# Performance work log

Hardware: AMD Instinct MI355X
Metric: run time of the kernel (lower is better)

Reference implementation:

```python
import jax, jax.numpy as jnp
import numpy as np

N = 100000   # nodes
E = 1600000  # edges
D = 128      # input_dim
H = 128      # hidden_dim
O = 128      # output_dim
G = 64       # graphs in batch
BN_EPS = 1e-5


def setup_inputs() -> dict:
    key = jax.random.key(0)
    ks = jax.random.split(key, 32)
    x = jax.random.normal(ks[0], (N, D), jnp.float32)
    edge_index = jax.random.randint(ks[1], (2, E), 0, N, dtype=jnp.int64)
    batch = jnp.sort(jax.random.randint(ks[2], (N,), 0, G, dtype=jnp.int64))

    def lin_w(k, fan_in, fan_out):
        return (jax.random.normal(k, (fan_in, fan_out), jnp.float32) / np.sqrt(fan_in)).astype(jnp.float32)

    def lin_b(k, fan_out):
        return (0.01 * jax.random.normal(k, (fan_out,), jnp.float32)).astype(jnp.float32)

    def bn(k, dim):
        k1, k2, k3, k4 = jax.random.split(k, 4)
        gamma = 1.0 + 0.1 * jax.random.normal(k1, (dim,), jnp.float32)
        beta = 0.1 * jax.random.normal(k2, (dim,), jnp.float32)
        mean = 0.1 * jax.random.normal(k3, (dim,), jnp.float32)
        var = 0.5 + jax.random.uniform(k4, (dim,), jnp.float32)
        return gamma, beta, mean, var

    inp = {
        "x": x, "edge_index": edge_index, "batch": batch,
        "w11": lin_w(ks[3], D, H), "b11": lin_b(ks[4], H),
        "w12": lin_w(ks[5], H, H), "b12": lin_b(ks[6], H),
        "w21": lin_w(ks[7], H, H), "b21": lin_b(ks[8], H),
        "w22": lin_w(ks[9], H, H), "b22": lin_b(ks[10], H),
        "w31": lin_w(ks[11], H, H), "b31": lin_b(ks[12], H),
        "w32": lin_w(ks[13], H, O), "b32": lin_b(ks[14], O),
    }
    g1, be1, m1, v1 = bn(ks[15], H)
    g2, be2, m2, v2 = bn(ks[16], H)
    g3, be3, m3, v3 = bn(ks[17], O)
    inp.update({"bn1_g": g1, "bn1_b": be1, "bn1_m": m1, "bn1_v": v1,
                "bn2_g": g2, "bn2_b": be2, "bn2_m": m2, "bn2_v": v2,
                "bn3_g": g3, "bn3_b": be3, "bn3_m": m3, "bn3_v": v3})
    return inp


def _gin_conv(x, src, dst, wa, ba, wb, bb):
    # sum-aggregate neighbor features: out[i] = x[i] + sum_{(j->i) in E} x[j]  (eps=0)
    agg = jax.ops.segment_sum(x[src], dst, num_segments=N)
    h = x + agg
    # 2-layer MLP: Linear -> ReLU -> Linear
    return jax.nn.relu(h @ wa + ba) @ wb + bb


def _bn_eval(x, g, b, m, v):
    return (x - m) * (g * jax.lax.rsqrt(v + BN_EPS)) + b


def reference(x, edge_index, batch,
              w11, b11, w12, b12, w21, b21, w22, b22, w31, b31, w32, b32,
              bn1_g, bn1_b, bn1_m, bn1_v,
              bn2_g, bn2_b, bn2_m, bn2_v,
              bn3_g, bn3_b, bn3_m, bn3_v):
    src, dst = edge_index[0], edge_index[1]
    h = _gin_conv(x, src, dst, w11, b11, w12, b12)
    h = jax.nn.relu(_bn_eval(h, bn1_g, bn1_b, bn1_m, bn1_v))  # dropout: eval-mode identity
    h = _gin_conv(h, src, dst, w21, b21, w22, b22)
    h = jax.nn.relu(_bn_eval(h, bn2_g, bn2_b, bn2_m, bn2_v))
    h = _gin_conv(h, src, dst, w31, b31, w32, b32)
    h = jax.nn.relu(_bn_eval(h, bn3_g, bn3_b, bn3_m, bn3_v))
    # global mean pool over each graph
    sums = jax.ops.segment_sum(h, batch, num_segments=G)
    counts = jax.ops.segment_sum(jnp.ones((N,), h.dtype), batch, num_segments=G)
    return sums / jnp.maximum(counts, 1.0)[:, None]
```

## Files before the change

kernel.cpp:

```cpp
#include <hip/hip_runtime.h>
#include <hip/hip_bf16.h>
#include <cstdint>

static constexpr int D = 128;
static constexpr int SPANB = 9;
static constexpr int CHUNK = 4096;

typedef __bf16 v8bf __attribute__((ext_vector_type(8)));
typedef float  v4f  __attribute__((ext_vector_type(4)));

__device__ inline float bflo(unsigned u) { return __uint_as_float(u << 16); }
__device__ inline float bfhi(unsigned u) { return __uint_as_float(u & 0xffff0000u); }
__device__ inline unsigned short bfbits(float f) {
    __hip_bfloat16 h = __float2bfloat16(f);
    return *reinterpret_cast<unsigned short*>(&h);
}
__device__ inline unsigned packbf(float a, float b) {
    return (unsigned)bfbits(a) | ((unsigned)bfbits(b) << 16);
}

__global__ __launch_bounds__(256) void prep_kernel(
    const float* __restrict__ w11, const float* __restrict__ w12,
    const float* __restrict__ w21, const float* __restrict__ w22,
    const float* __restrict__ w31, const float* __restrict__ w32,
    __hip_bfloat16* __restrict__ Wp,
    const float* bn1g, const float* bn1b, const float* bn1m, const float* bn1v, const float* lb1,
    const float* bn2g, const float* bn2b, const float* bn2m, const float* bn2v, const float* lb2,
    const float* bn3g, const float* bn3b, const float* bn3m, const float* bn3v, const float* lb3,
    float* sc1, float* sh1, float* sc2, float* sh2, float* sc3, float* sh3,
    const float* __restrict__ x, __hip_bfloat16* __restrict__ xb, long long n8,
    const int* __restrict__ dst, int* __restrict__ blockhist, int nE, int nblk) {
    int b = blockIdx.x, t = threadIdx.x;
    if (b < 48) {
        int idx = b * 256 + t;
        int widx = idx >> 11, r = idx & 2047;
        const float* W = widx == 0 ? w11 : widx == 1 ? w12 : widx == 2 ? w21
                       : widx == 3 ? w22 : widx == 4 ? w31 : w32;
        int l = r & 63, cf = (r >> 6) & 7, ks = r >> 9;
        int k0 = ks * 32 + (l >> 4) * 8, c = cf * 16 + (l & 15);
        unsigned o0 = packbf(W[(k0 + 0) * D + c], W[(k0 + 1) * D + c]);
        unsigned o1 = packbf(W[(k0 + 2) * D + c], W[(k0 + 3) * D + c]);
        unsigned o2 = packbf(W[(k0 + 4) * D + c], W[(k0 + 5) * D + c]);
        unsigned o3 = packbf(W[(k0 + 6) * D + c], W[(k0 + 7) * D + c]);
        reinterpret_cast<uint4*>(Wp + (size_t)idx * 8)[0] = make_uint4(o0, o1, o2, o3);
    } else if (b < 51) {
        if (t < D) {
            int j = b - 48;
            const float *g, *bb, *m, *v, *lb;
            float *sc, *sh;
            if (j == 0)      { g = bn1g; bb = bn1b; m = bn1m; v = bn1v; lb = lb1; sc = sc1; sh = sh1; }
            else if (j == 1) { g = bn2g; bb = bn2b; m = bn2m; v = bn2v; lb = lb2; sc = sc2; sh = sh2; }
            else             { g = bn3g; bb = bn3b; m = bn3m; v = bn3v; lb = lb3; sc = sc3; sh = sh3; }
            float s = g[t] * rsqrtf(v[t] + 1e-5f);
            sc[t] = s;
            sh[t] = (lb[t] - m[t]) * s + bb[t];
        }
    } else if (b < 51 + nblk) {
        __shared__ int h[256];
        h[t] = 0;
        __syncthreads();
        int base = (b - 51) * CHUNK;
#pragma unroll
        for (int i = 0; i < CHUNK / 256; ++i) {
            int e = base + i * 256 + t;
            if (e < nE) atomicAdd(&h[dst[e] >> SPANB], 1);
        }
        __syncthreads();
        blockhist[(b - 51) * 256 + t] = h[t];
    } else {
        long long i = (long long)(b - 51 - nblk) * 256 + t;
        if (i < n8) {
            const float4* f4 = reinterpret_cast<const float4*>(x);
            float4 a = f4[i * 2], bb = f4[i * 2 + 1];
            uint4 o = make_uint4(packbf(a.x, a.y), packbf(a.z, a.w),
                                 packbf(bb.x, bb.y), packbf(bb.z, bb.w));
            reinterpret_cast<uint4*>(xb)[i] = o;
        }
    }
}

__global__ __launch_bounds__(256) void bscan_kernel(int* __restrict__ blockhist,
                                                    int* __restrict__ totals, int nblk) {
    __shared__ int s[256];
    int b = blockIdx.x, t = threadIdx.x;
    int running = 0;
    for (int base = 0; base < nblk; base += 256) {
        int idx = base + t;
        int v = (idx < nblk) ? blockhist[idx * 256 + b] : 0;
        s[t] = v;
        __syncthreads();
#pragma unroll
        for (int off = 1; off < 256; off <<= 1) {
            int add = (t >= off) ? s[t - off] : 0;
            __syncthreads();
            s[t] += add;
            __syncthreads();
        }
        if (idx < nblk) blockhist[idx * 256 + b] = running + s[t] - v;
        int tot = s[255];
        __syncthreads();
        running += tot;
    }
    if (t == 0) totals[b] = running;
}

__global__ void tscan_kernel(const int* __restrict__ totals,
                             int* __restrict__ bucketbase, int nbuk, int nE) {
    __shared__ int s[256];
    int t = threadIdx.x;
    int v = (t < nbuk) ? totals[t] : 0;
    s[t] = v;
    __syncthreads();
#pragma unroll
    for (int off = 1; off < 256; off <<= 1) {
        int add = (t >= off) ? s[t - off] : 0;
        __syncthreads();
        s[t] += add;
        __syncthreads();
    }
    if (t < nbuk) bucketbase[t] = s[t] - v;
    if (t == 0) bucketbase[nbuk] = nE;
}

__global__ __launch_bounds__(256) void fill2_kernel(const int* __restrict__ src,
                                                    const int* __restrict__ dst,
                                                    const int* __restrict__ blockhist,
                                                    const int* __restrict__ bucketbase,
                                                    unsigned* __restrict__ records,
                                                    int nE, int nbuk) {
    __shared__ int cur[256];
    int t = threadIdx.x;
    if (t < nbuk) cur[t] = bucketbase[t] + blockhist[blockIdx.x * 256 + t];
    __syncthreads();
    int base = blockIdx.x * CHUNK;
#pragma unroll
    for (int i = 0; i < CHUNK / 256; ++i) {
        int e = base + i * 256 + t;
        if (e < nE) {
            int d = dst[e], s = src[e];
            int p = atomicAdd(&cur[d >> SPANB], 1);
            records[p] = ((unsigned)s << SPANB) | (unsigned)(d & ((1 << SPANB) - 1));
        }
    }
}

__global__ __launch_bounds__(512) void csr2_kernel(const unsigned* __restrict__ records,
                                                   const int* __restrict__ bucketbase,
                                                   int* __restrict__ rowptr,
                                                   int* __restrict__ col,
                                                   int nN, int nE) {
    __shared__ int cnt[512];
    __shared__ int cur[512];
    int b = blockIdx.x, t = threadIdx.x;
    int node0 = b << SPANB;
    cnt[t] = 0;
    __syncthreads();
    int rbeg = bucketbase[b], rend = bucketbase[b + 1];
    for (int r = rbeg + t; r < rend; r += 512)
        atomicAdd(&cnt[records[r] & ((1 << SPANB) - 1)], 1);
    __syncthreads();
    int v = cnt[t];
#pragma unroll
    for (int off = 1; off < 512; off <<= 1) {
        int add = (t >= off) ? cnt[t - off] : 0;
        __syncthreads();
        cnt[t] += add;
        __syncthreads();
    }
    int pos = rbeg + cnt[t] - v;
    if (node0 + t < nN) rowptr[node0 + t] = pos;
    if (b == 0 && t == 0) rowptr[nN] = nE;
    cur[t] = pos;
    __syncthreads();
    for (int r = rbeg + t; r < rend; r += 512) {
        unsigned rec = records[r];
        int p = atomicAdd(&cur[rec & ((1 << SPANB) - 1)], 1);
        col[p] = (int)(rec >> SPANB);
    }
}

#define ACC8(vv) { a[0]+=bflo(vv.x); a[1]+=bfhi(vv.x); a[2]+=bflo(vv.y); a[3]+=bfhi(vv.y); \
                   a[4]+=bflo(vv.z); a[5]+=bfhi(vv.z); a[6]+=bflo(vv.w); a[7]+=bfhi(vv.w); }

__global__ __launch_bounds__(256) void agg_kernel(const __hip_bfloat16* __restrict__ h,
                                                  __hip_bfloat16* __restrict__ S,
                                                  const int* __restrict__ rowptr,
                                                  const int* __restrict__ col, int nN) {
    int node = blockIdx.x * 16 + (threadIdx.x >> 4);
    if (node >= nN) return;
    int q = threadIdx.x & 15;
    const uint4* h4 = reinterpret_cast<const uint4*>(h);
    uint4 u = h4[(size_t)node * 16 + q];
    float a[8];
    a[0] = bflo(u.x); a[1] = bfhi(u.x); a[2] = bflo(u.y); a[3] = bfhi(u.y);
    a[4] = bflo(u.z); a[5] = bfhi(u.z); a[6] = bflo(u.w); a[7] = bfhi(u.w);
    int beg = rowptr[node], end = rowptr[node + 1];
    int j = beg;
    for (; j + 3 < end; j += 4) {
        int s0 = col[j], s1 = col[j + 1], s2 = col[j + 2], s3 = col[j + 3];
        uint4 v0 = h4[(size_t)s0 * 16 + q];
        uint4 v1 = h4[(size_t)s1 * 16 + q];
        uint4 v2 = h4[(size_t)s2 * 16 + q];
        uint4 v3 = h4[(size_t)s3 * 16 + q];
        ACC8(v0); ACC8(v1); ACC8(v2); ACC8(v3);
    }
    for (; j < end; ++j) {
        uint4 v0 = h4[(size_t)col[j] * 16 + q];
        ACC8(v0);
    }
    uint4 o = make_uint4(packbf(a[0], a[1]), packbf(a[2], a[3]),
                         packbf(a[4], a[5]), packbf(a[6], a[7]));
    reinterpret_cast<uint4*>(S)[(size_t)node * 16 + q] = o;
}

__global__ __launch_bounds__(256) void mlp_fused_kernel(
    const __hip_bfloat16* __restrict__ A,
    const __hip_bfloat16* __restrict__ WpA,
    const __hip_bfloat16* __restrict__ WpB,
    const float* __restrict__ b1,
    const float* __restrict__ sc, const float* __restrict__ sh,
    __hip_bfloat16* __restrict__ out, int nN) {
    __shared__ __attribute__((aligned(16))) char smem[4][8192];
    int w = threadIdx.x >> 6, l = threadIdx.x & 63;
    int q = l >> 4, r16 = l & 15;
    int row0 = blockIdx.x * 128 + w * 32;
    int rowA = row0 + r16, rowB = row0 + 16 + r16;
    int arA = rowA < nN ? rowA : nN - 1;
    int arB = rowB < nN ? rowB : nN - 1;
    const v8bf* ArA = reinterpret_cast<const v8bf*>(A + (size_t)arA * D);
    const v8bf* ArB = reinterpret_cast<const v8bf*>(A + (size_t)arB * D);
    const v8bf* Wa = reinterpret_cast<const v8bf*>(WpA);
    const v8bf* Wb = reinterpret_cast<const v8bf*>(WpB);
    const float4* b14 = reinterpret_cast<const float4*>(b1);
    const float4* sc4 = reinterpret_cast<const float4*>(sc);
    const float4* sh4 = reinterpret_cast<const float4*>(sh);
    char* my = smem[w];
    int swz = (r16 & 7) << 4;

    v4f acc[2][8] = {};
#pragma unroll
    for (int ks = 0; ks < 4; ++ks) {
        v8bf bA = ArA[ks * 4 + q];
        v8bf bB = ArB[ks * 4 + q];
#pragma unroll
        for (int cf = 0; cf < 8; ++cf) {
            v8bf wa = Wa[(ks * 8 + cf) * 64 + l];
            acc[0][cf] = __builtin_amdgcn_mfma_f32_16x16x32_bf16(wa, bA, acc[0][cf], 0, 0, 0);
            acc[1][cf] = __builtin_amdgcn_mfma_f32_16x16x32_bf16(wa, bB, acc[1][cf], 0, 0, 0);
        }
    }
#pragma unroll
    for (int half = 0; half < 2; ++half) {
        char* base = my + half * 4096;
#pragma unroll
        for (int cf = 0; cf < 8; ++cf) {
            float4 bb = b14[cf * 4 + q];
            float e0 = fmaxf(acc[half][cf][0] + bb.x, 0.f);
            float e1 = fmaxf(acc[half][cf][1] + bb.y, 0.f);
            float e2 = fmaxf(acc[half][cf][2] + bb.z, 0.f);
            float e3 = fmaxf(acc[half][cf][3] + bb.w, 0.f);
            int waddr = r16 * 256 + ((cf * 32 + q * 8) ^ swz);
            *reinterpret_cast<uint2*>(base + waddr) = make_uint2(packbf(e0, e1), packbf(e2, e3));
        }
    }
    __syncthreads();

    v4f acc2[2][8] = {};
#pragma unroll
    for (int ks = 0; ks < 4; ++ks) {
        v8bf bA = *reinterpret_cast<v8bf*>(my + r16 * 256 + ((ks * 64 + q * 16) ^ swz));
        v8bf bB = *reinterpret_cast<v8bf*>(my + 4096 + r16 * 256 + ((ks * 64 + q * 16) ^ swz));
#pragma unroll
        for (int cf = 0; cf < 8; ++cf) {
            v8bf wb = Wb[(ks * 8 + cf) * 64 + l];
            acc2[0][cf] = __builtin_amdgcn_mfma_f32_16x16x32_bf16(wb, bA, acc2[0][cf], 0, 0, 0);
            acc2[1][cf] = __builtin_amdgcn_mfma_f32_16x16x32_bf16(wb, bB, acc2[1][cf], 0, 0, 0);
        }
    }
#pragma unroll
    for (int half = 0; half < 2; ++half) {
        int row = (half == 0) ? rowA : rowB;
        if (row < nN) {
#pragma unroll
            for (int cf = 0; cf < 8; ++cf) {
                float4 s0 = sc4[cf * 4 + q], s1 = sh4[cf * 4 + q];
                float e0 = fmaxf(acc2[half][cf][0] * s0.x + s1.x, 0.f);
                float e1 = fmaxf(acc2[half][cf][1] * s0.y + s1.y, 0.f);
                float e2 = fmaxf(acc2[half][cf][2] * s0.z + s1.z, 0.f);
                float e3 = fmaxf(acc2[half][cf][3] * s0.w + s1.w, 0.f);
                *reinterpret_cast<uint2*>(out + (size_t)row * D + cf * 16 + q * 4) =
                    make_uint2(packbf(e0, e1), packbf(e2, e3));
            }
        }
    }
}

__global__ __launch_bounds__(1024) void pool2_kernel(const __hip_bfloat16* __restrict__ h,
                                                     const int* __restrict__ batch,
                                                     float* __restrict__ out, int nN) {
    int g = blockIdx.x;
    int lo, hi;
    {
        int a = 0, b = nN;
        while (a < b) { int mid = (a + b) >> 1; if (batch[mid] < g) a = mid + 1; else b = mid; }
        lo = a;
        b = nN;
        while (a < b) { int mid = (a + b) >> 1; if (batch[mid] < g + 1) a = mid + 1; else b = mid; }
        hi = a;
    }
    int grp = threadIdx.x >> 4;
    int q = threadIdx.x & 15;
    float a[8] = {};
    const uint4* h4 = reinterpret_cast<const uint4*>(h);
    for (int i = lo + grp; i < hi; i += 64) {
        uint4 v = h4[(size_t)i * 16 + q];
        ACC8(v);
    }
    __shared__ float red[64][130];
#pragma unroll
    for (int k = 0; k < 8; ++k) red[grp][q * 8 + k] = a[k];
    __syncthreads();
    int t = threadIdx.x;
    if (t < D) {
        float s = 0.f;
#pragma unroll 8
        for (int r = 0; r < 64; ++r) s += red[r][t];
        out[(size_t)g * D + t] = s / fmaxf((float)(hi - lo), 1.f);
    }
}

extern "C" void kernel_launch(void* const* d_in, const int* in_sizes, int n_in,
                              void* d_out, int out_size, void* d_ws, size_t ws_size,
                              hipStream_t stream) {
    const float* x    = (const float*)d_in[0];
    const int*   ei   = (const int*)d_in[1];
    const int*   batch= (const int*)d_in[2];
    const float* w11 = (const float*)d_in[3];  const float* b11 = (const float*)d_in[4];
    const float* w12 = (const float*)d_in[5];  const float* b12 = (const float*)d_in[6];
    const float* w21 = (const float*)d_in[7];  const float* b21 = (const float*)d_in[8];
    const float* w22 = (const float*)d_in[9];  const float* b22 = (const float*)d_in[10];
    const float* w31 = (const float*)d_in[11]; const float* b31 = (const float*)d_in[12];
    const float* w32 = (const float*)d_in[13]; const float* b32 = (const float*)d_in[14];
    const float* bn1g = (const float*)d_in[15]; const float* bn1b = (const float*)d_in[16];
    const float* bn1m = (const float*)d_in[17]; const float* bn1v = (const float*)d_in[18];
    const float* bn2g = (const float*)d_in[19]; const float* bn2b = (const float*)d_in[20];
    const float* bn2m = (const float*)d_in[21]; const float* bn2v = (const float*)d_in[22];
    const float* bn3g = (const float*)d_in[23]; const float* bn3b = (const float*)d_in[24];
    const float* bn3m = (const float*)d_in[25]; const float* bn3v = (const float*)d_in[26];

    int nN = in_sizes[0] / D;
    int nE = in_sizes[1] / 2;
    int nG = out_size / D;

    const int* srcp = ei;
    const int* dstp = ei + nE;

    size_t NB2 = (size_t)nN * D * sizeof(__hip_bfloat16);
    char* ws = (char*)d_ws;
    __hip_bfloat16* S16 = (__hip_bfloat16*)ws;
    __hip_bfloat16* M16 = (__hip_bfloat16*)(ws + NB2);
    __hip_bfloat16* P16 = (__hip_bfloat16*)(ws + 2 * NB2);
    __hip_bfloat16* Wp  = (__hip_bfloat16*)(ws + 3 * NB2);
    size_t wp_bytes = 6 * 2048 * 8 * sizeof(__hip_bfloat16);
    char* auxp = ws + 3 * NB2 + wp_bytes;
    size_t aux_bytes = 16384;
    float* sc1 = (float*)auxp + 0,   *sh1 = (float*)auxp + 128;
    float* sc2 = (float*)auxp + 256, *sh2 = (float*)auxp + 384;
    float* sc3 = (float*)auxp + 512, *sh3 = (float*)auxp + 640;
    int*   bucketbase = (int*)(auxp + (768 + 64) * 4);
    int*   totals     = bucketbase + 300;
    int* rowptr = (int*)(auxp + aux_bytes);
    int* col    = rowptr + (nN + 1);

    unsigned* records = (unsigned*)M16;
    int* blockhist    = (int*)((char*)M16 + (size_t)nE * 4);

    int nbuk = (nN + 511) >> SPANB;
    int nblk = (nE + CHUNK - 1) / CHUNK;
    long long n8 = (long long)nN * D / 8;
    int cvtBlocks = (int)((n8 + 255) / 256);

    prep_kernel<<<51 + nblk + cvtBlocks, 256, 0, stream>>>(
        w11, w12, w21, w22, w31, w32, Wp,
        bn1g, bn1b, bn1m, bn1v, b12,
        bn2g, bn2b, bn2m, bn2v, b22,
        bn3g, bn3b, bn3m, bn3v, b32,
        sc1, sh1, sc2, sh2, sc3, sh3,
        x, (__hip_bfloat16*)P16, n8,
        dstp, blockhist, nE, nblk);

    bscan_kernel<<<nbuk, 256, 0, stream>>>(blockhist, totals, nblk);
    tscan_kernel<<<1, 256, 0, stream>>>(totals, bucketbase, nbuk, nE);
    fill2_kernel<<<nblk, 256, 0, stream>>>(srcp, dstp, blockhist, bucketbase, records, nE, nbuk);
    csr2_kernel<<<nbuk, 512, 0, stream>>>(records, bucketbase, rowptr, col, nN, nE);

    int mlpBlocks = (nN + 127) / 128;
    int aggBlocks = (nN + 15) / 16;
    __hip_bfloat16* Wp1 = Wp + 0 * 16384; __hip_bfloat16* Wp2 = Wp + 1 * 16384;
    __hip_bfloat16* Wp3 = Wp + 2 * 16384; __hip_bfloat16* Wp4 = Wp + 3 * 16384;
    __hip_bfloat16* Wp5 = Wp + 4 * 16384; __hip_bfloat16* Wp6 = Wp + 5 * 16384;

    agg_kernel<<<aggBlocks, 256, 0, stream>>>(P16, S16, rowptr, col, nN);
    mlp_fused_kernel<<<mlpBlocks, 256, 0, stream>>>(S16, Wp1, Wp2, b11, sc1, sh1, P16, nN);

    agg_kernel<<<aggBlocks, 256, 0, stream>>>(P16, S16, rowptr, col, nN);
    mlp_fused_kernel<<<mlpBlocks, 256, 0, stream>>>(S16, Wp3, Wp4, b21, sc2, sh2, P16, nN);

    agg_kernel<<<aggBlocks, 256, 0, stream>>>(P16, S16, rowptr, col, nN);
    mlp_fused_kernel<<<mlpBlocks, 256, 0, stream>>>(S16, Wp5, Wp6, b31, sc3, sh3, P16, nN);

    pool2_kernel<<<nG, 1024, 0, stream>>>(P16, batch, (float*)d_out, nN);
}
```

Baseline: 346.6 us.

## Fuse neighbor aggregation and MLP into one per-layer kernel via LDS

Merges the gather-sum aggregation kernel and the two-layer MLP kernel into one layer kernel. Each block aggregates 64 nodes into swizzled shared memory, then runs both MFMA GEMMs on that tile, so the aggregated bf16 tensor is never written to or reread from global memory. The cost is fewer rows per wave (16 instead of 32), which halves weight-fragment reuse, plus extra barriers. The gather phase also now shares a block with MFMA work, which could lower the number of loads in flight.

```diff
diff --git a/kernel.cpp b/kernel.cpp
--- a/kernel.cpp
+++ b/kernel.cpp
@@ -182,115 +182,109 @@
 #define ACC8(vv) { a[0]+=bflo(vv.x); a[1]+=bfhi(vv.x); a[2]+=bflo(vv.y); a[3]+=bfhi(vv.y); \
                    a[4]+=bflo(vv.z); a[5]+=bfhi(vv.z); a[6]+=bflo(vv.w); a[7]+=bfhi(vv.w); }
 
-__global__ __launch_bounds__(256) void agg_kernel(const __hip_bfloat16* __restrict__ h,
-                                                  __hip_bfloat16* __restrict__ S,
-                                                  const int* __restrict__ rowptr,
-                                                  const int* __restrict__ col, int nN) {
-    int node = blockIdx.x * 16 + (threadIdx.x >> 4);
-    if (node >= nN) return;
-    int q = threadIdx.x & 15;
-    const uint4* h4 = reinterpret_cast<const uint4*>(h);
-    uint4 u = h4[(size_t)node * 16 + q];
-    float a[8];
-    a[0] = bflo(u.x); a[1] = bfhi(u.x); a[2] = bflo(u.y); a[3] = bfhi(u.y);
-    a[4] = bflo(u.z); a[5] = bfhi(u.z); a[6] = bflo(u.w); a[7] = bfhi(u.w);
-    int beg = rowptr[node], end = rowptr[node + 1];
-    int j = beg;
-    for (; j + 3 < end; j += 4) {
-        int s0 = col[j], s1 = col[j + 1], s2 = col[j + 2], s3 = col[j + 3];
-        uint4 v0 = h4[(size_t)s0 * 16 + q];
-        uint4 v1 = h4[(size_t)s1 * 16 + q];
-        uint4 v2 = h4[(size_t)s2 * 16 + q];
-        uint4 v3 = h4[(size_t)s3 * 16 + q];
-        ACC8(v0); ACC8(v1); ACC8(v2); ACC8(v3);
-    }
-    for (; j < end; ++j) {
-        uint4 v0 = h4[(size_t)col[j] * 16 + q];
-        ACC8(v0);
-    }
-    uint4 o = make_uint4(packbf(a[0], a[1]), packbf(a[2], a[3]),
-                         packbf(a[4], a[5]), packbf(a[6], a[7]));
-    reinterpret_cast<uint4*>(S)[(size_t)node * 16 + q] = o;
-}
-
-__global__ __launch_bounds__(256) void mlp_fused_kernel(
-    const __hip_bfloat16* __restrict__ A,
-    const __hip_bfloat16* __restrict__ WpA,
-    const __hip_bfloat16* __restrict__ WpB,
+__global__ __launch_bounds__(256) void layer_kernel(
+    const __hip_bfloat16* __restrict__ Hin,
+    const int* __restrict__ rowptr, const int* __restrict__ col,
+    const __hip_bfloat16* __restrict__ WpA, const __hip_bfloat16* __restrict__ WpB,
     const float* __restrict__ b1,
     const float* __restrict__ sc, const float* __restrict__ sh,
-    __hip_bfloat16* __restrict__ out, int nN) {
-    __shared__ __attribute__((aligned(16))) char smem[4][8192];
-    int w = threadIdx.x >> 6, l = threadIdx.x & 63;
-    int q = l >> 4, r16 = l & 15;
-    int row0 = blockIdx.x * 128 + w * 32;
-    int rowA = row0 + r16, rowB = row0 + 16 + r16;
-    int arA = rowA < nN ? rowA : nN - 1;
-    int arB = rowB < nN ? rowB : nN - 1;
-    const v8bf* ArA = reinterpret_cast<const v8bf*>(A + (size_t)arA * D);
-    const v8bf* ArB = reinterpret_cast<const v8bf*>(A + (size_t)arB * D);
+    __hip_bfloat16* __restrict__ Hout, int nN) {
+    __shared__ __attribute__((aligned(16))) char Sl[64 * 256];
+    int t = threadIdx.x;
+    int row0 = blockIdx.x * 64;
+
+    {
+        int grp = t >> 4, q = t & 15;
+        const uint4* h4 = reinterpret_cast<const uint4*>(Hin);
+#pragma unroll
+        for (int n = 0; n < 4; ++n) {
+            int r = grp * 4 + n;
+            int node = row0 + r;
+            int waddr = r * 256 + ((q * 16) ^ ((r & 7) << 4));
+            if (node >= nN) {
+                *reinterpret_cast<uint4*>(Sl + waddr) = make_uint4(0, 0, 0, 0);
+                continue;
+            }
+            uint4 u = h4[(size_t)node * 16 + q];
+            float a[8];
+            a[0] = bflo(u.x); a[1] = bfhi(u.x); a[2] = bflo(u.y); a[3] = bfhi(u.y);
+            a[4] = bflo(u.z); a[5] = bfhi(u.z); a[6] = bflo(u.w); a[7] = bfhi(u.w);
+            int beg = rowptr[node], end = rowptr[node + 1];
+            int j = beg;
+            for (; j + 3 < end; j += 4) {
+                int s0 = col[j], s1 = col[j + 1], s2 = col[j + 2], s3 = col[j + 3];
+                uint4 v0 = h4[(size_t)s0 * 16 + q];
+                uint4 v1 = h4[(size_t)s1 * 16 + q];
+                uint4 v2 = h4[(size_t)s2 * 16 + q];
+                uint4 v3 = h4[(size_t)s3 * 16 + q];
+                ACC8(v0); ACC8(v1); ACC8(v2); ACC8(v3);
+            }
+            for (; j < end; ++j) {
+                uint4 v0 = h4[(size_t)col[j] * 16 + q];
+                ACC8(v0);
+            }
+            *reinterpret_cast<uint4*>(Sl + waddr) =
+                make_uint4(packbf(a[0], a[1]), packbf(a[2], a[3]),
+                           packbf(a[4], a[5]), packbf(a[6], a[7]));
+        }
+    }
+    __syncthreads();
+
+    int w = t >> 6, l = t & 63;
+    int q2 = l >> 4, r16 = l & 15;
+    int lrow = w * 16 + r16;
+    int row = row0 + lrow;
+    int swz = (r16 & 7) << 4;
+    char* srow = Sl + lrow * 256;
+    char* mid = Sl + w * 4096;
     const v8bf* Wa = reinterpret_cast<const v8bf*>(WpA);
     const v8bf* Wb = reinterpret_cast<const v8bf*>(WpB);
     const float4* b14 = reinterpret_cast<const float4*>(b1);
     const float4* sc4 = reinterpret_cast<const float4*>(sc);
     const float4* sh4 = reinterpret_cast<const float4*>(sh);
-    char* my = smem[w];
-    int swz = (r16 & 7) << 4;
-
-    v4f acc[2][8] = {};
+
+    v4f acc[8] = {};
 #pragma unroll
     for (int ks = 0; ks < 4; ++ks) {
-        v8bf bA = ArA[ks * 4 + q];
-        v8bf bB = ArB[ks * 4 + q];
+        v8bf bfrag = *reinterpret_cast<v8bf*>(srow + (((ks * 4 + q2) * 16) ^ swz));
+#pragma unroll
+        for (int cf = 0; cf < 8; ++cf)
+            acc[cf] = __builtin_amdgcn_mfma_f32_16x16x32_bf16(
+                Wa[(ks * 8 + cf) * 64 + l], bfrag, acc[cf], 0, 0, 0);
+    }
+    __syncthreads();
+
+#pragma unroll
+    for (int cf = 0; cf < 8; ++cf) {
+        float4 bb = b14[cf * 4 + q2];
+        float e0 = fmaxf(acc[cf][0] + bb.x, 0.f);
+        float e1 = fmaxf(acc[cf][1] + bb.y, 0.f);
+        float e2 = fmaxf(acc[cf][2] + bb.z, 0.f);
+        float e3 = fmaxf(acc[cf][3] + bb.w, 0.f);
+        int waddr = r16 * 256 + ((cf * 32 + q2 * 8) ^ swz);
+        *reinterpret_cast<uint2*>(mid + waddr) = make_uint2(packbf(e0, e1), packbf(e2, e3));
+    }
+    __syncthreads();
+
+    v4f acc2[8] = {};
+#pragma unroll
+    for (int ks = 0; ks < 4; ++ks) {
+        v8bf bfrag = *reinterpret_cast<v8bf*>(mid + r16 * 256 + ((ks * 64 + q2 * 16) ^ swz));
+#pragma unroll
+        for (int cf = 0; cf < 8; ++cf)
+            acc2[cf] = __builtin_amdgcn_mfma_f32_16x16x32_bf16(
+                Wb[(ks * 8 + cf) * 64 + l], bfrag, acc2[cf], 0, 0, 0);
+    }
+    if (row < nN) {
 #pragma unroll
         for (int cf = 0; cf < 8; ++cf) {
-            v8bf wa = Wa[(ks * 8 + cf) * 64 + l];
-            acc[0][cf] = __builtin_amdgcn_mfma_f32_16x16x32_bf16(wa, bA, acc[0][cf], 0, 0, 0);
-            acc[1][cf] = __builtin_amdgcn_mfma_f32_16x16x32_bf16(wa, bB, acc[1][cf], 0, 0, 0);
-        }
-    }
-#pragma unroll
-    for (int half = 0; half < 2; ++half) {
-        char* base = my + half * 4096;
-#pragma unroll
-        for (int cf = 0; cf < 8; ++cf) {
-            float4 bb = b14[cf * 4 + q];
-            float e0 = fmaxf(acc[half][cf][0] + bb.x, 0.f);
-            float e1 = fmaxf(acc[half][cf][1] + bb.y, 0.f);
-            float e2 = fmaxf(acc[half][cf][2] + bb.z, 0.f);
-            float e3 = fmaxf(acc[half][cf][3] + bb.w, 0.f);
-            int waddr = r16 * 256 + ((cf * 32 + q * 8) ^ swz);
-            *reinterpret_cast<uint2*>(base + waddr) = make_uint2(packbf(e0, e1), packbf(e2, e3));
-        }
-    }
-    __syncthreads();
-
-    v4f acc2[2][8] = {};
-#pragma unroll
-    for (int ks = 0; ks < 4; ++ks) {
-        v8bf bA = *reinterpret_cast<v8bf*>(my + r16 * 256 + ((ks * 64 + q * 16) ^ swz));
-        v8bf bB = *reinterpret_cast<v8bf*>(my + 4096 + r16 * 256 + ((ks * 64 + q * 16) ^ swz));
-#pragma unroll
-        for (int cf = 0; cf < 8; ++cf) {
-            v8bf wb = Wb[(ks * 8 + cf) * 64 + l];
-            acc2[0][cf] = __builtin_amdgcn_mfma_f32_16x16x32_bf16(wb, bA, acc2[0][cf], 0, 0, 0);
-            acc2[1][cf] = __builtin_amdgcn_mfma_f32_16x16x32_bf16(wb, bB, acc2[1][cf], 0, 0, 0);
-        }
-    }
-#pragma unroll
-    for (int half = 0; half < 2; ++half) {
-        int row = (half == 0) ? rowA : rowB;
-        if (row < nN) {
-#pragma unroll
-            for (int cf = 0; cf < 8; ++cf) {
-                float4 s0 = sc4[cf * 4 + q], s1 = sh4[cf * 4 + q];
-                float e0 = fmaxf(acc2[half][cf][0] * s0.x + s1.x, 0.f);
-                float e1 = fmaxf(acc2[half][cf][1] * s0.y + s1.y, 0.f);
-                float e2 = fmaxf(acc2[half][cf][2] * s0.z + s1.z, 0.f);
-                float e3 = fmaxf(acc2[half][cf][3] * s0.w + s1.w, 0.f);
-                *reinterpret_cast<uint2*>(out + (size_t)row * D + cf * 16 + q * 4) =
-                    make_uint2(packbf(e0, e1), packbf(e2, e3));
-            }
+            float4 s0 = sc4[cf * 4 + q2], s1 = sh4[cf * 4 + q2];
+            float e0 = fmaxf(acc2[cf][0] * s0.x + s1.x, 0.f);
+            float e1 = fmaxf(acc2[cf][1] * s0.y + s1.y, 0.f);
+            float e2 = fmaxf(acc2[cf][2] * s0.z + s1.z, 0.f);
+            float e3 = fmaxf(acc2[cf][3] * s0.w + s1.w, 0.f);
+            *reinterpret_cast<uint2*>(Hout + (size_t)row * D + cf * 16 + q2 * 4) =
+                make_uint2(packbf(e0, e1), packbf(e2, e3));
         }
     }
 }
@@ -357,12 +351,11 @@
 
     size_t NB2 = (size_t)nN * D * sizeof(__hip_bfloat16);
     char* ws = (char*)d_ws;
-    __hip_bfloat16* S16 = (__hip_bfloat16*)ws;
-    __hip_bfloat16* M16 = (__hip_bfloat16*)(ws + NB2);
-    __hip_bfloat16* P16 = (__hip_bfloat16*)(ws + 2 * NB2);
-    __hip_bfloat16* Wp  = (__hip_bfloat16*)(ws + 3 * NB2);
+    __hip_bfloat16* A16 = (__hip_bfloat16*)ws;
+    __hip_bfloat16* B16 = (__hip_bfloat16*)(ws + NB2);
+    __hip_bfloat16* Wp  = (__hip_bfloat16*)(ws + 2 * NB2);
     size_t wp_bytes = 6 * 2048 * 8 * sizeof(__hip_bfloat16);
-    char* auxp = ws + 3 * NB2 + wp_bytes;
+    char* auxp = ws + 2 * NB2 + wp_bytes;
     size_t aux_bytes = 16384;
     float* sc1 = (float*)auxp + 0,   *sh1 = (float*)auxp + 128;
     float* sc2 = (float*)auxp + 256, *sh2 = (float*)auxp + 384;
@@ -372,8 +365,8 @@
     int* rowptr = (int*)(auxp + aux_bytes);
     int* col    = rowptr + (nN + 1);
 
-    unsigned* records = (unsigned*)M16;
-    int* blockhist    = (int*)((char*)M16 + (size_t)nE * 4);
+    unsigned* records = (unsigned*)B16;
+    int* blockhist    = (int*)((char*)B16 + (size_t)nE * 4);
 
     int nbuk = (nN + 511) >> SPANB;
     int nblk = (nE + CHUNK - 1) / CHUNK;
@@ -386,7 +379,7 @@
         bn2g, bn2b, bn2m, bn2v, b22,
         bn3g, bn3b, bn3m, bn3v, b32,
         sc1, sh1, sc2, sh2, sc3, sh3,
-        x, (__hip_bfloat16*)P16, n8,
+        x, A16, n8,
         dstp, blockhist, nE, nblk);
 
     bscan_kernel<<<nbuk, 256, 0, stream>>>(blockhist, totals, nblk);
@@ -394,20 +387,14 @@
     fill2_kernel<<<nblk, 256, 0, stream>>>(srcp, dstp, blockhist, bucketbase, records, nE, nbuk);
     csr2_kernel<<<nbuk, 512, 0, stream>>>(records, bucketbase, rowptr, col, nN, nE);
 
-    int mlpBlocks = (nN + 127) / 128;
-    int aggBlocks = (nN + 15) / 16;
+    int layerBlocks = (nN + 63) / 64;
     __hip_bfloat16* Wp1 = Wp + 0 * 16384; __hip_bfloat16* Wp2 = Wp + 1 * 16384;
     __hip_bfloat16* Wp3 = Wp + 2 * 16384; __hip_bfloat16* Wp4 = Wp + 3 * 16384;
     __hip_bfloat16* Wp5 = Wp + 4 * 16384; __hip_bfloat16* Wp6 = Wp + 5 * 16384;
 
-    agg_kernel<<<aggBlocks, 256, 0, stream>>>(P16, S16, rowptr, col, nN);
-    mlp_fused_kernel<<<mlpBlocks, 256, 0, stream>>>(S16, Wp1, Wp2, b11, sc1, sh1, P16, nN);
-
-    agg_kernel<<<aggBlocks, 256, 0, stream>>>(P16, S16, rowptr, col, nN);
-    mlp_fused_kernel<<<mlpBlocks, 256, 0, stream>>>(S16, Wp3, Wp4, b21, sc2, sh2, P16, nN);
-
-    agg_kernel<<<aggBlocks, 256, 0, stream>>>(P16, S16, rowptr, col, nN);
-    mlp_fused_kernel<<<mlpBlocks, 256, 0, stream>>>(S16, Wp5, Wp6, b31, sc3, sh3, P16, nN);
-
-    pool2_kernel<<<nG, 1024, 0, stream>>>(P16, batch, (float*)d_out, nN);
-}
+    layer_kernel<<<layerBlocks, 256, 0, stream>>>(A16, rowptr, col, Wp1, Wp2, b11, sc1, sh1, B16, nN);
+    layer_kernel<<<layerBlocks, 256, 0, stream>>>(B16, rowptr, col, Wp3, Wp4, b21, sc2, sh2, A16, nN);
+    layer_kernel<<<layerBlocks, 256, 0, stream>>>(A16, rowptr, col, Wp5, Wp6, b31, sc3, sh3, B16, nN);
+
+    pool2_kernel<<<nG, 1024, 0, stream>>>(B16, batch, (float*)d_out, nN);
+}
```

New measurement: 330.3 us. 1.05x faster.
